# Performance work log

Hardware: AMD Instinct MI355X
Metric: run time of the kernel (lower is better)

The kernel has to match this reference:

```python
import jax, jax.numpy as jnp
import numpy as np

N = 10000        # nodes
F_IN = 128       # node features (data.num_node_features)
OUT = 16         # out_channels
H = 32           # attention heads
C1 = 4 * OUT     # hidden per-head dim (4*out_channels)
E = 80000        # directed edges
EPS = 1e-5       # BatchNorm eps
NEG = 0.2        # GATConv LeakyReLU negative_slope


def _gat(x, src, dst, W, a_s, a_d, b, n, C):
    # PyG GATConv, shared lin, concat=False (mean over heads)
    h = (x @ W).reshape(n, H, C)                    # [n,H,C]
    e_src = jnp.sum(h * a_s, -1)                    # [n,H] (alpha from x_j)
    e_dst = jnp.sum(h * a_d, -1)                    # [n,H] (alpha from x_i)
    e = jax.nn.leaky_relu(e_src[src] + e_dst[dst], NEG)     # [E',H]
    m = jax.ops.segment_max(e, dst, num_segments=n)         # segment softmax
    p = jnp.exp(e - m[dst])
    z = jax.ops.segment_sum(p, dst, num_segments=n)
    alpha = p / z[dst]
    out = jax.ops.segment_sum(alpha[:, :, None] * h[src], dst, num_segments=n)
    return out.mean(1) + b                          # mean over heads + bias


def _bn(x, g, b, m, v):  # eval-mode BatchNorm1d (running stats)
    return (x - m) * g / jnp.sqrt(v + EPS) + b


def setup_inputs():
    k = jax.random.split(jax.random.key(0), 40)
    rn = lambda i, s, sc=0.1: jax.random.normal(k[i], s, jnp.float32) * sc
    d = {"x": jax.random.normal(k[0], (N, F_IN), jnp.float32),
         "edge_index": jax.random.randint(k[1], (2, E), 0, N, jnp.int32)}
    # 4 GATConv layers
    d.update(W1=rn(2, (F_IN, H * C1)), as1=rn(3, (H, C1)), ad1=rn(4, (H, C1)), b1=rn(5, (C1,)))
    d.update(W2=rn(6, (C1, H * OUT)), as2=rn(7, (H, OUT)), ad2=rn(8, (H, OUT)), b2=rn(9, (OUT,)))
    d.update(W3=rn(10, (F_IN, H * C1)), as3=rn(11, (H, C1)), ad3=rn(12, (H, C1)), b3=rn(13, (C1,)))
    d.update(W4=rn(14, (C1, H * OUT)), as4=rn(15, (H, OUT)), ad4=rn(16, (H, OUT)), b4=rn(17, (OUT,)))
    # ResidualNetwork(1 block): 1x1 Conv1d over L=1 == matmul
    d.update(rwa=rn(18, (F_IN, OUT)), rba=rn(19, (OUT,)),
             bn1g=jnp.ones(OUT), bn1b=jnp.zeros(OUT), bn1m=rn(20, (OUT,)), bn1v=jnp.abs(rn(21, (OUT,))) + 1.0,
             rwb=rn(22, (OUT, OUT)), rbb=rn(23, (OUT,)),
             bn2g=jnp.ones(OUT), bn2b=jnp.zeros(OUT), bn2m=rn(24, (OUT,)), bn2v=jnp.abs(rn(25, (OUT,))) + 1.0,
             wsc=rn(26, (F_IN, OUT)), bsc=rn(27, (OUT,)),
             bnsg=jnp.ones(OUT), bnsb=jnp.zeros(OUT), bnsm=rn(28, (OUT,)), bnsv=jnp.abs(rn(29, (OUT,))) + 1.0,
             wfc=rn(30, (OUT, OUT)), bfc=rn(31, (OUT,)))
    return d


def reference(x, edge_index, W1, as1, ad1, b1, W2, as2, ad2, b2,
              W3, as3, ad3, b3, W4, as4, ad4, b4,
              rwa, rba, bn1g, bn1b, bn1m, bn1v, rwb, rbb, bn2g, bn2b, bn2m, bn2v,
              wsc, bsc, bnsg, bnsb, bnsm, bnsv, wfc, bfc):
    n = x.shape[0]
    loops = jnp.arange(n, dtype=edge_index.dtype)  # add_self_loops=True
    s2t_src = jnp.concatenate([edge_index[0], loops])  # flow source_to_target
    s2t_dst = jnp.concatenate([edge_index[1], loops])
    t2s_src = jnp.concatenate([edge_index[1], loops])  # flow target_to_source
    t2s_dst = jnp.concatenate([edge_index[0], loops])
    # dropout in original is unassigned (no-op); eval mode assumed
    x_s = jax.nn.elu(_gat(x, s2t_src, s2t_dst, W1, as1, ad1, b1, n, C1))
    x_in = jax.nn.elu(_gat(x_s, s2t_src, s2t_dst, W2, as2, ad2, b2, n, OUT))
    x_t = jax.nn.elu(_gat(x, t2s_src, t2s_dst, W3, as3, ad3, b3, n, C1))
    x_out = jax.nn.elu(_gat(x_t, t2s_src, t2s_dst, W4, as4, ad4, b4, n, OUT))
    # ResidualNetwork: block + identity avg-pool (L=1) + fc
    h = jax.nn.relu(_bn(x @ rwa + rba, bn1g, bn1b, bn1m, bn1v))
    h = _bn(h @ rwb + rbb, bn2g, bn2b, bn2m, bn2v)
    sc = _bn(x @ wsc + bsc, bnsg, bnsb, bnsm, bnsv)
    x_self = jax.nn.relu(h + sc) @ wfc + bfc
    return (x_in, x_out, x_self)
```

## Files before the change

### kernel.cpp

```cpp
#include <hip/hip_runtime.h>
#include <stdint.h>

__device__ __forceinline__ float bf2f(unsigned short u) {
  union { unsigned int i; float f; } v; v.i = ((unsigned int)u) << 16; return v.f;
}
__device__ __forceinline__ unsigned short f2bf(float f) {
  union { float f; unsigned int i; } v; v.f = f;
  unsigned int i = v.i;
  unsigned int r = (i + 0x7fffu + ((i >> 16) & 1u)) >> 16;
  return (unsigned short)r;
}

typedef __bf16 bf16x8 __attribute__((ext_vector_type(8)));
typedef float f32x4 __attribute__((ext_vector_type(4)));
typedef float f32x2 __attribute__((ext_vector_type(2)));
union ABfrag { int4 i4; bf16x8 v; };

#if __has_builtin(__builtin_amdgcn_cvt_pk_fp8_f32) && __has_builtin(__builtin_amdgcn_cvt_pk_f32_fp8)
#define HW_FP8 1
#else
#define HW_FP8 0
#endif

__device__ __forceinline__ unsigned char f2fp8_sw(float f) {
  union { float f; unsigned int u; } v; v.f = f;
  unsigned int s = (v.u >> 24) & 0x80;
  float a = fabsf(f);
  if (a >= 448.f) return (unsigned char)(s | 0x7E);
  v.f = a;
  int ex = (int)(v.u >> 23);
  unsigned int man = v.u & 0x7FFFFFu;
  if (ex >= 121) {
    unsigned int val = ((unsigned int)(ex - 120) << 3) | (man >> 20);
    unsigned int rem = man & 0xFFFFFu;
    if (rem > 0x80000u || (rem == 0x80000u && (val & 1))) val++;
    if (val > 0x7E) val = 0x7E;
    return (unsigned char)(s | val);
  }
  int q = (int)(a * 512.f + 0.5f);
  if (q > 8) q = 8;
  return (unsigned char)(s | (unsigned int)q);
}
__device__ __forceinline__ float fp8dec_sw(unsigned char c) {
  unsigned int e = (c >> 3) & 15u, m = c & 7u;
  float v;
  if (e) { union { unsigned int u; float f; } x; x.u = ((e + 120) << 23) | (m << 20); v = x.f; }
  else v = (float)m * 0.001953125f;
  return (c & 0x80) ? -v : v;
}
__device__ __forceinline__ unsigned int pack4_fp8(float a0, float a1, float a2, float a3) {
#if HW_FP8
  int dw = __builtin_amdgcn_cvt_pk_fp8_f32(a0, a1, 0, false);
  dw = __builtin_amdgcn_cvt_pk_fp8_f32(a2, a3, dw, true);
  return (unsigned int)dw;
#else
  return (unsigned)f2fp8_sw(a0) | ((unsigned)f2fp8_sw(a1) << 8) |
         ((unsigned)f2fp8_sw(a2) << 16) | ((unsigned)f2fp8_sw(a3) << 24);
#endif
}
__device__ __forceinline__ unsigned int bytesel4(uint4 v, int rr) {
#if __has_builtin(__builtin_amdgcn_perm)
  unsigned s = (unsigned)rr | ((unsigned)(rr + 4) << 8);
  unsigned p01 = __builtin_amdgcn_perm(v.y, v.x, s);
  unsigned p23 = __builtin_amdgcn_perm(v.w, v.z, s);
  return __builtin_amdgcn_perm(p23, p01, 0x05040100u);
#else
  int sh = rr * 8;
  return ((v.x >> sh) & 0xFFu) | (((v.y >> sh) & 0xFFu) << 8) |
         (((v.z >> sh) & 0xFFu) << 16) | (((v.w >> sh) & 0xFFu) << 24);
#endif
}
__device__ __forceinline__ void dec16p(int4 g, f32x2 o[8]) {
#if HW_FP8
  o[0] = __builtin_amdgcn_cvt_pk_f32_fp8(g.x, false);
  o[1] = __builtin_amdgcn_cvt_pk_f32_fp8(g.x, true);
  o[2] = __builtin_amdgcn_cvt_pk_f32_fp8(g.y, false);
  o[3] = __builtin_amdgcn_cvt_pk_f32_fp8(g.y, true);
  o[4] = __builtin_amdgcn_cvt_pk_f32_fp8(g.z, false);
  o[5] = __builtin_amdgcn_cvt_pk_f32_fp8(g.z, true);
  o[6] = __builtin_amdgcn_cvt_pk_f32_fp8(g.w, false);
  o[7] = __builtin_amdgcn_cvt_pk_f32_fp8(g.w, true);
#else
  unsigned int w[4] = {(unsigned)g.x, (unsigned)g.y, (unsigned)g.z, (unsigned)g.w};
#pragma unroll
  for (int d = 0; d < 4; ++d) {
    unsigned int x = w[d];
    o[d * 2 + 0] = (f32x2){fp8dec_sw((unsigned char)(x & 0xFF)),
                           fp8dec_sw((unsigned char)((x >> 8) & 0xFF))};
    o[d * 2 + 1] = (f32x2){fp8dec_sw((unsigned char)((x >> 16) & 0xFF)),
                           fp8dec_sw((unsigned char)((x >> 24) & 0xFF))};
  }
#endif
}

__device__ __forceinline__ float lrelu_clamp(float e) {
  e = (e > 0.f) ? e : 0.2f * e;
  return fminf(e, 80.f);
}

__global__ __launch_bounds__(256) void k_detect(const unsigned int* __restrict__ x, int* flag,
                                                int* __restrict__ degAB, int ndeg2) {
  if (blockIdx.x == 0) {
    __shared__ int cnt;
    if (threadIdx.x == 0) cnt = 0;
    __syncthreads();
    int c = 0;
    for (int i = threadIdx.x; i < 1024; i += 256) {
      unsigned int lo = x[i] & 0xFFFFu;
      int ex = (int)((lo >> 7) & 0xFF);
      if (ex >= 100 && ex <= 140) c++;
    }
    atomicAdd(&cnt, c);
    __syncthreads();
    if (threadIdx.x == 0) flag[0] = (cnt > 600) ? 1 : 0;
    return;
  }
  for (int idx = (blockIdx.x - 1) * 256 + threadIdx.x; idx < ndeg2; idx += 8 * 256) degAB[idx] = 0;
}

struct PrepDesc {
  const void* csrc[32]; float* cdst[32]; int cn[32];
  const void* x; float* xc; unsigned short* xp;
  const void* W1; const void* W2; const void* W3; const void* W4;
  unsigned short* P1; unsigned short* P2; unsigned short* P3; unsigned short* P4;
  int* degAB;
  const int* ei;
  const void* av[4];
  float* wa[4];
  int nxb, xtotal, ctotal, E, nn;
};
__global__ __launch_bounds__(256) void k_prep(PrepDesc d, const int* __restrict__ flag) {
  int isbf = *flag;
  int b = blockIdx.x;
  if (b < d.nxb) {
    int t8 = b * 256 + threadIdx.x;
    int i8 = t8 * 8;
    if (i8 < d.xtotal) {
      float v[8];
      if (isbf) {
        int4 raw = *(const int4*)((const unsigned short*)d.x + i8);
        const unsigned short* u = (const unsigned short*)&raw;
#pragma unroll
        for (int j = 0; j < 8; ++j) v[j] = bf2f(u[j]);
      } else {
        float4 f0 = *(const float4*)((const float*)d.x + i8);
        float4 f1 = *(const float4*)((const float*)d.x + i8 + 4);
        v[0] = f0.x; v[1] = f0.y; v[2] = f0.z; v[3] = f0.w;
        v[4] = f1.x; v[5] = f1.y; v[6] = f1.z; v[7] = f1.w;
      }
      *(float4*)(d.xc + i8)     = (float4){v[0], v[1], v[2], v[3]};
      *(float4*)(d.xc + i8 + 4) = (float4){v[4], v[5], v[6], v[7]};
      int row = i8 >> 7, c0 = i8 & 127;
      int tm = row >> 4, mr = row & 15;
      int s = c0 >> 5, quad = (c0 >> 3) & 3;
      unsigned short o[8];
#pragma unroll
      for (int j = 0; j < 8; ++j) o[j] = f2bf(v[j]);
      size_t idx = (((size_t)tm * 4 + s) * 64 + quad * 16 + mr) * 8;
      *(int4*)(d.xp + idx) = *(const int4*)o;
    }
    return;
  }
  b -= d.nxb;
  if (b < 288) {
    int u = b * 256 + threadIdx.x;
    const void* W; unsigned short* P; int K, N, lu;
    if (u < 32768)      { W = d.W1; P = d.P1; K = 128; N = 2048; lu = u; }
    else if (u < 36864) { W = d.W2; P = d.P2; K = 64;  N = 512;  lu = u - 32768; }
    else if (u < 69632) { W = d.W3; P = d.P3; K = 128; N = 2048; lu = u - 36864; }
    else                { W = d.W4; P = d.P4; K = 64;  N = 512;  lu = u - 69632; }
    int ksteps = K >> 5;
    int g = lu / (ksteps * 64);
    int rem = lu - g * (ksteps * 64);
    int s = rem >> 6, lane = rem & 63;
    int mr = lane & 15, quad = lane >> 4;
    int col = g * 16 + mr;
    int kbase = s * 32 + quad * 8;
#pragma unroll
    for (int j = 0; j < 8; ++j) {
      size_t src = (size_t)(kbase + j) * N + col;
      float v = isbf ? bf2f(((const unsigned short*)W)[src]) : ((const float*)W)[src];
      P[(size_t)lu * 8 + j] = f2bf(v);
    }
    return;
  }
  b -= 288;
  if (b < 4) {
    for (int idx = b * 256 + threadIdx.x; idx < d.ctotal; idx += 4 * 256) {
      int t = 0, off = idx;
      while (off >= d.cn[t]) { off -= d.cn[t]; ++t; }
      float v = isbf ? bf2f(((const unsigned short*)d.csrc[t])[off])
                     : ((const float*)d.csrc[t])[off];
      d.cdst[t][off] = v;
    }
    return;
  }
  b -= 4;
  {
    int degblks = (d.E + 255) >> 8;
    if (b < degblks) {
      int e = b * 256 + threadIdx.x;
      if (e < d.E) {
        atomicAdd(&d.degAB[d.ei[d.E + e]], 1);
        atomicAdd(&d.degAB[d.nn + d.ei[e]], 1);
      }
      return;
    }
    b -= degblks;
  }
  {
    int m = b >> 4, kb = b & 15;
    const void* W = (m < 2) ? d.W1 : d.W3;
    const void* A = d.av[m];
    float* out = d.wa[m];
    int k = kb * 8 + (threadIdx.x >> 5);
    int h = threadIdx.x & 31;
    size_t wbase = (size_t)k * 2048 + h * 64;
    size_t abase = (size_t)h * 64;
    float acc = 0.f;
    if (isbf) {
      const unsigned short* Wb = (const unsigned short*)W;
      const unsigned short* Ab = (const unsigned short*)A;
#pragma unroll
      for (int v8 = 0; v8 < 8; ++v8) {
        int4 wv = *(const int4*)(Wb + wbase + v8 * 8);
        int4 av = *(const int4*)(Ab + abase + v8 * 8);
        const unsigned short* wu = (const unsigned short*)&wv;
        const unsigned short* au = (const unsigned short*)&av;
#pragma unroll
        for (int j = 0; j < 8; ++j) acc += bf2f(wu[j]) * bf2f(au[j]);
      }
    } else {
      const float* Wf = (const float*)W;
      const float* Af = (const float*)A;
#pragma unroll
      for (int v4 = 0; v4 < 16; ++v4) {
        float4 wv = *(const float4*)(Wf + wbase + v4 * 4);
        float4 av = *(const float4*)(Af + abase + v4 * 4);
        acc += wv.x * av.x + wv.y * av.y + wv.z * av.z + wv.w * av.w;
      }
    }
    out[k * 32 + h] = acc;
  }
}

__global__ __launch_bounds__(1024) void k_exscan2(const int* __restrict__ degA, const int* __restrict__ degB,
                                                  int* __restrict__ rowA, int* __restrict__ rowB,
                                                  int* __restrict__ colA, int* __restrict__ colB,
                                                  int* __restrict__ curA, int* __restrict__ curB, int n) {
  const int* deg = (blockIdx.x == 0) ? degA : degB;
  int* row = (blockIdx.x == 0) ? rowA : rowB;
  int* colx = (blockIdx.x == 0) ? colA : colB;
  int* curx = (blockIdx.x == 0) ? curA : curB;
  __shared__ int wsum[16], wbase[16];
  __shared__ int carry;
  if (threadIdx.x == 0) carry = 0;
  __syncthreads();
  int lane = threadIdx.x & 63, w = threadIdx.x >> 6;
  int chunks = (n + 1023) >> 10;
  for (int ch = 0; ch < chunks; ++ch) {
    int i = (ch << 10) + threadIdx.x;
    int v = (i < n) ? deg[i] : 0;
    int sc = v;
#pragma unroll
    for (int o = 1; o < 64; o <<= 1) { int t = __shfl_up(sc, o); if (lane >= o) sc += t; }
    if (lane == 63) wsum[w] = sc;
    __syncthreads();
    if (threadIdx.x < 16) {
      int v2 = wsum[threadIdx.x], s2 = v2;
#pragma unroll
      for (int o = 1; o < 16; o <<= 1) { int t = __shfl_up(s2, o); if (lane >= o) s2 += t; }
      wbase[threadIdx.x] = s2 - v2;
      if (threadIdx.x == 15) wsum[15] = s2;
    }
    __syncthreads();
    if (i < n) {
      int rv = carry + wbase[w] + (sc - v) + i;
      row[i] = rv;
      colx[rv] = i;
      curx[i] = rv + 1;
    }
    __syncthreads();
    if (threadIdx.x == 0) carry += wsum[15];
    __syncthreads();
  }
  if (threadIdx.x == 0) row[n] = carry + n;
}

struct AuxDesc {
  int resblks, E;
  const int* ei; int* colA; int* colB; int* curA; int* curB;
  const float* xc;
  const float* rp[20];
  const float* wa[4];
  float* es1; float* ed1; float* es3; float* ed3;
  void* outbase; size_t eoff; int n;
  const int* flag;
};
__global__ __launch_bounds__(256) void k_aux(AuxDesc d) {
  __shared__ struct { float xs[16][128]; float ha[16][16]; float tt[16][16]; } sm;
  int b = blockIdx.x;
  if (b < d.resblks) {
    int nodebase = b * 16;
    for (int t = threadIdx.x; t < 16 * 128; t += 256)
      sm.xs[t >> 7][t & 127] = d.xc[(size_t)(nodebase + (t >> 7)) * 128 + (t & 127)];
    __syncthreads();
    int ni = threadIdx.x >> 4, c = threadIdx.x & 15;
    {
      const float* w0 = d.wa[0]; const float* w1 = d.wa[1];
      const float* w2 = d.wa[2]; const float* w3 = d.wa[3];
      float a0 = 0.f, a1 = 0.f, a2 = 0.f, a3 = 0.f, a4 = 0.f, a5 = 0.f, a6 = 0.f, a7 = 0.f;
#pragma unroll 4
      for (int k = 0; k < 128; ++k) {
        float xv = sm.xs[ni][k];
        int o = k * 32 + c;
        a0 += xv * w0[o]; a1 += xv * w0[o + 16];
        a2 += xv * w1[o]; a3 += xv * w1[o + 16];
        a4 += xv * w2[o]; a5 += xv * w2[o + 16];
        a6 += xv * w3[o]; a7 += xv * w3[o + 16];
      }
      int row = nodebase + ni;
      d.es1[row * 32 + c] = a0; d.es1[row * 32 + c + 16] = a1;
      d.ed1[row * 32 + c] = a2; d.ed1[row * 32 + c + 16] = a3;
      d.es3[row * 32 + c] = a4; d.es3[row * 32 + c + 16] = a5;
      d.ed3[row * 32 + c] = a6; d.ed3[row * 32 + c + 16] = a7;
    }
    const float* rwa = d.rp[0]; const float* rba = d.rp[1];
    const float* bn1g = d.rp[2]; const float* bn1b = d.rp[3];
    const float* bn1m = d.rp[4]; const float* bn1v = d.rp[5];
    const float* rwb = d.rp[6]; const float* rbb = d.rp[7];
    const float* bn2g = d.rp[8]; const float* bn2b = d.rp[9];
    const float* bn2m = d.rp[10]; const float* bn2v = d.rp[11];
    const float* wsc = d.rp[12]; const float* bsc = d.rp[13];
    const float* bnsg = d.rp[14]; const float* bnsb = d.rp[15];
    const float* bnsm = d.rp[16]; const float* bnsv = d.rp[17];
    const float* wfc = d.rp[18]; const float* bfc = d.rp[19];
    float ya = 0.f, ysc = 0.f;
#pragma unroll 8
    for (int k = 0; k < 128; ++k) {
      float xv = sm.xs[ni][k];
      ya  += xv * rwa[k * 16 + c];
      ysc += xv * wsc[k * 16 + c];
    }
    ya += rba[c]; ysc += bsc[c];
    float s1 = bn1g[c] * rsqrtf(bn1v[c] + 1e-5f);
    ya = (ya - bn1m[c]) * s1 + bn1b[c];
    ya = fmaxf(ya, 0.f);
    float ss = bnsg[c] * rsqrtf(bnsv[c] + 1e-5f);
    ysc = (ysc - bnsm[c]) * ss + bnsb[c];
    sm.ha[ni][c] = ya;
    __syncthreads();
    float h2 = rbb[c];
#pragma unroll
    for (int k = 0; k < 16; ++k) h2 += sm.ha[ni][k] * rwb[k * 16 + c];
    float s2 = bn2g[c] * rsqrtf(bn2v[c] + 1e-5f);
    h2 = (h2 - bn2m[c]) * s2 + bn2b[c];
    sm.tt[ni][c] = fmaxf(h2 + ysc, 0.f);
    __syncthreads();
    float o = bfc[c];
#pragma unroll
    for (int k = 0; k < 16; ++k) o += sm.tt[ni][k] * wfc[k * 16 + c];
    size_t oo = d.eoff + (size_t)(nodebase + ni) * 16 + c;
    if (*d.flag) ((unsigned short*)d.outbase)[oo] = f2bf(o);
    else         ((float*)d.outbase)[oo] = o;
    return;
  }
  b -= d.resblks;
  {
    int e = b * 256 + threadIdx.x;
    if (e < d.E) {
      int s = d.ei[e], dd = d.ei[d.E + e];
      d.colA[atomicAdd(&d.curA[dd], 1)] = s;
      d.colB[atomicAdd(&d.curB[s], 1)] = dd;
    }
  }
}

#define TILE_DW 288
template<int CH, int KSTEPS>
__device__ __forceinline__ void mm_es64_body(int rg, int cg, int MT,
    const unsigned short* __restrict__ Ap, const unsigned short* __restrict__ Bp,
    unsigned char* __restrict__ C, const float* __restrict__ a_s, const float* __restrict__ a_d,
    float* __restrict__ es, float* __restrict__ ed, int N, unsigned int* tile) {
  const int TI = KSTEPS * 64;
  int vt = MT - rg * 4; if (vt > 4) vt = 4;
  int wid = threadIdx.x >> 6;
  int tn = cg * 4 + wid;
  int lane = threadIdx.x & 63;
  int mr = lane & 15, quad = lane >> 4;
  const int4* ap = (const int4*)(Ap + (size_t)rg * 4 * TI * 8) + lane;
  const unsigned short* bp = Bp + ((size_t)tn * 4 * KSTEPS) * 512 + lane * 8;
  unsigned int* twave = tile + wid * TILE_DW;
  f32x4 acc[4][4];
#pragma unroll
  for (int rt = 0; rt < 4; ++rt)
#pragma unroll
    for (int nt = 0; nt < 4; ++nt) acc[rt][nt] = (f32x4){0.f, 0.f, 0.f, 0.f};
#pragma unroll
  for (int s = 0; s < KSTEPS; ++s) {
    ABfrag bfr[4];
#pragma unroll
    for (int nt = 0; nt < 4; ++nt) bfr[nt].i4 = *(const int4*)(bp + (size_t)(nt * KSTEPS + s) * 512);
    ABfrag afr[4];
#pragma unroll
    for (int rt = 0; rt < 4; ++rt) {
      int rti = (rt < vt) ? rt : 0;
      afr[rt].i4 = ap[rti * TI + s * 64];
    }
#pragma unroll
    for (int nt = 0; nt < 4; ++nt)
#pragma unroll
      for (int rt = 0; rt < 4; ++rt)
        acc[rt][nt] = __builtin_amdgcn_mfma_f32_16x16x32_bf16(afr[rt].v, bfr[nt].v, acc[rt][nt], 0, 0, 0);
  }
  int r16 = lane >> 2, seg = lane & 3;
  int qr = r16 >> 2, rr = r16 & 3;
#pragma unroll
  for (int rt = 0; rt < 4; ++rt) {
    if (rt < vt) {
      int tm = rg * 4 + rt;
#pragma unroll
      for (int nt = 0; nt < 4; ++nt) {
        unsigned int dwv = pack4_fp8(acc[rt][nt][0], acc[rt][nt][1], acc[rt][nt][2], acc[rt][nt][3]);
        twave[quad * 72 + nt * 16 + mr] = dwv;
      }
      unsigned int out[4];
#pragma unroll
      for (int w = 0; w < 4; ++w) {
        uint4 v = *(const uint4*)&twave[qr * 72 + seg * 16 + 4 * w];
        out[w] = bytesel4(v, rr);
      }
      *(int4*)(C + (size_t)(tm * 16 + r16) * N + tn * 64 + seg * 16) = *(const int4*)out;
    }
  }
  if (CH == 16) {
    float ws[4], wd[4];
#pragma unroll
    for (int nt = 0; nt < 4; ++nt) {
      ws[nt] = a_s[(tn * 4 + nt) * 16 + mr];
      wd[nt] = a_d[(tn * 4 + nt) * 16 + mr];
    }
#pragma unroll
    for (int rt = 0; rt < 4; ++rt) {
      if (rt < vt) {
        int tm = rg * 4 + rt;
        float pes[4][4], ped[4][4];
#pragma unroll
        for (int nt = 0; nt < 4; ++nt)
#pragma unroll
          for (int r = 0; r < 4; ++r) { pes[nt][r] = acc[rt][nt][r] * ws[nt]; ped[nt][r] = acc[rt][nt][r] * wd[nt]; }
#pragma unroll
        for (int m = 1; m < 16; m <<= 1)
#pragma unroll
          for (int nt = 0; nt < 4; ++nt)
#pragma unroll
            for (int r = 0; r < 4; ++r) {
              pes[nt][r] += __shfl_xor(pes[nt][r], m);
              ped[nt][r] += __shfl_xor(ped[nt][r], m);
            }
        if (mr == 0) {
#pragma unroll
          for (int nt = 0; nt < 4; ++nt)
#pragma unroll
            for (int r = 0; r < 4; ++r) {
              int row = tm * 16 + quad * 4 + r;
              es[row * 32 + tn * 4 + nt] = pes[nt][r];
              ed[row * 32 + tn * 4 + nt] = ped[nt][r];
            }
        }
      }
    }
  }
}

struct MMDesc {
  const unsigned short* Ap;
  const unsigned short* B1; const unsigned short* B3;
  unsigned char* C1; unsigned char* C3;
  int mmblks, mt;
};
__global__ __launch_bounds__(256) void k_mm13(MMDesc d) {
  __shared__ unsigned int tile[4 * TILE_DW];
  int b = blockIdx.x;
  if (b < d.mmblks) {
    mm_es64_body<64,4>(b >> 3, b & 7, d.mt, d.Ap, d.B1, d.C1, nullptr, nullptr, nullptr, nullptr, 2048, tile);
    return;
  }
  b -= d.mmblks;
  mm_es64_body<64,4>(b >> 3, b & 7, d.mt, d.Ap, d.B3, d.C3, nullptr, nullptr, nullptr, nullptr, 2048, tile);
}

__global__ __launch_bounds__(256) void k_g64(const unsigned char* __restrict__ h1,
                                             const unsigned char* __restrict__ h3,
                                             const float* __restrict__ es1, const float* __restrict__ ed1,
                                             const float* __restrict__ es3, const float* __restrict__ ed3,
                                             const int* __restrict__ rowA, const int* __restrict__ colA,
                                             const int* __restrict__ rowB, const int* __restrict__ colB,
                                             const float* __restrict__ b1, const float* __restrict__ b3,
                                             unsigned short* __restrict__ xsp, unsigned short* __restrict__ xtp,
                                             int n, int gb) {
  int b = blockIdx.x;
  const unsigned char* h; const float *es, *ed, *bias; const int *rowp, *col; unsigned short* outp;
  if (b < gb) { h = h1; es = es1; ed = ed1; rowp = rowA; col = colA; bias = b1; outp = xsp; }
  else { b -= gb; h = h3; es = es3; ed = ed3; rowp = rowB; col = colB; bias = b3; outp = xtp; }
  int wid = threadIdx.x >> 6, lane = threadIdx.x & 63;
  int i = b * 4 + wid;
  if (i >= n) return;
  int hd0 = lane >> 2, hd1 = 16 + hd0;
  float e0 = ed[i * 32 + hd0];
  float e1 = ed[i * 32 + hd1];
  int beg = rowp[i], end = rowp[i + 1];
  int deg = end - beg;
  int colv = (lane < deg) ? col[beg + lane] : 0;
  f32x2 acc0[8], acc1[8];
#pragma unroll
  for (int k = 0; k < 8; ++k) { acc0[k] = (f32x2){0.f, 0.f}; acc1[k] = (f32x2){0.f, 0.f}; }
  float Z0 = 0.f, Z1 = 0.f;
  int s0 = __shfl(colv, 0);
  const int4* hp0 = (const int4*)(h + (size_t)s0 * 2048);
  int4 ng0 = hp0[lane];
  int4 ng1 = hp0[64 + lane];
  float na = es[s0 * 32 + hd0];
  float nb = es[s0 * 32 + hd1];
  for (int j = 0; j < deg; ++j) {
    int4 g0 = ng0, g1 = ng1;
    float ea = na, eb = nb;
    int jn = j + 1;
    if (jn < deg) {
      int sn = (jn < 64) ? __shfl(colv, jn) : col[beg + jn];
      const int4* hq = (const int4*)(h + (size_t)sn * 2048);
      ng0 = hq[lane];
      ng1 = hq[64 + lane];
      na = es[sn * 32 + hd0];
      nb = es[sn * 32 + hd1];
    }
    float q0 = __expf(lrelu_clamp(ea + e0));
    float q1 = __expf(lrelu_clamp(eb + e1));
    Z0 += q0; Z1 += q1;
    f32x2 d0[8], d1[8];
    dec16p(g0, d0); dec16p(g1, d1);
    f32x2 q0v = (f32x2){q0, q0}, q1v = (f32x2){q1, q1};
#pragma unroll
    for (int k = 0; k < 8; ++k) {
      acc0[k] = __builtin_elementwise_fma(q0v, d0[k], acc0[k]);
      acc1[k] = __builtin_elementwise_fma(q1v, d1[k], acc1[k]);
    }
  }
  float zi0 = 1.0f / Z0, zi1 = 1.0f / Z1;
  f32x2 zi0v = (f32x2){zi0, zi0}, zi1v = (f32x2){zi1, zi1};
  f32x2 v2[8];
#pragma unroll
  for (int k = 0; k < 8; ++k)
    v2[k] = __builtin_elementwise_fma(acc1[k], zi1v, acc0[k] * zi0v);
#pragma unroll
  for (int m = 4; m < 64; m <<= 1)
#pragma unroll
    for (int k = 0; k < 8; ++k) {
      v2[k].x += __shfl_xor(v2[k].x, m);
      v2[k].y += __shfl_xor(v2[k].y, m);
    }
  if (lane < 4) {
    float v[16];
#pragma unroll
    for (int k = 0; k < 8; ++k) { v[2 * k] = v2[k].x; v[2 * k + 1] = v2[k].y; }
    int tm = i >> 4, mr = i & 15;
    unsigned short ob[16];
#pragma unroll
    for (int k = 0; k < 16; ++k) {
      float t = v[k] * (1.f / 32.f) + bias[lane * 16 + k];
      t = (t > 0.f) ? t : (__expf(t) - 1.f);
      ob[k] = f2bf(t);
    }
    int s0w = lane >> 1;
#pragma unroll
    for (int g2 = 0; g2 < 2; ++g2) {
      size_t idx = (((size_t)tm * 2 + s0w) * 64 + ((lane & 1) * 2 + g2) * 16 + mr) * 8;
      *(int4*)(outp + idx) = *(const int4*)(ob + g2 * 8);
    }
  }
}

__global__ __launch_bounds__(256) void k_mm24(const unsigned short* __restrict__ xsp,
                                              const unsigned short* __restrict__ xtp,
                                              const unsigned short* __restrict__ W2p,
                                              const unsigned short* __restrict__ W4p,
                                              unsigned char* __restrict__ h2, unsigned char* __restrict__ h4,
                                              const float* __restrict__ as2, const float* __restrict__ ad2,
                                              const float* __restrict__ as4, const float* __restrict__ ad4,
                                              float* __restrict__ es2, float* __restrict__ ed2,
                                              float* __restrict__ es4, float* __restrict__ ed4,
                                              int mmblks, int mt) {
  __shared__ unsigned int tile[4 * TILE_DW];
  int b = blockIdx.x;
  if (b < mmblks)
    mm_es64_body<16,2>(b >> 1, b & 1, mt, xsp, W2p, h2, as2, ad2, es2, ed2, 512, tile);
  else {
    b -= mmblks;
    mm_es64_body<16,2>(b >> 1, b & 1, mt, xtp, W4p, h4, as4, ad4, es4, ed4, 512, tile);
  }
}

__global__ __launch_bounds__(256) void k_g16(const unsigned char* __restrict__ h2,
                                             const unsigned char* __restrict__ h4,
                                             const float* __restrict__ es2, const float* __restrict__ ed2,
                                             const float* __restrict__ es4, const float* __restrict__ ed4,
                                             const int* __restrict__ rowA, const int* __restrict__ colA,
                                             const int* __restrict__ rowB, const int* __restrict__ colB,
                                             const float* __restrict__ b2, const float* __restrict__ b4,
                                             void* __restrict__ outbase, int n, int gb,
                                             const int* __restrict__ flag) {
  int b = blockIdx.x;
  const unsigned char* h; const float *es, *ed, *bias; const int *rowp, *col; size_t eoff;
  if (b < gb) { h = h2; es = es2; ed = ed2; rowp = rowA; col = colA; bias = b2; eoff = 0; }
  else { b -= gb; h = h4; es = es4; ed = ed4; rowp = rowB; col = colB; bias = b4; eoff = (size_t)n * 16; }
  int wid = threadIdx.x >> 6, lane = threadIdx.x & 63;
  int i = b * 4 + wid;
  if (i >= n) return;
  int hh = lane & 31, j2 = lane >> 5;
  float ev = ed[i * 32 + hh];
  int beg = rowp[i], end = rowp[i + 1];
  int deg = end - beg;
  int colv = (lane < deg) ? col[beg + lane] : 0;
  f32x2 acc[8];
#pragma unroll
  for (int k = 0; k < 8; ++k) acc[k] = (f32x2){0.f, 0.f};
  float Z = 0.f;
  int j = j2;
  int4 ng = (int4){0, 0, 0, 0};
  float ne = 0.f;
  if (j < deg) {
    int s = __shfl(colv, j);
    ng = ((const int4*)(h + (size_t)s * 512))[hh];
    ne = es[s * 32 + hh];
  }
  for (; j < deg; j += 2) {
    int4 g = ng; float ee = ne;
    int jn = j + 2;
    if (jn < deg) {
      int sn = (jn < 64) ? __shfl(colv, jn) : col[beg + jn];
      ng = ((const int4*)(h + (size_t)sn * 512))[hh];
      ne = es[sn * 32 + hh];
    }
    float q = __expf(lrelu_clamp(ee + ev));
    Z += q;
    f32x2 d[8];
    dec16p(g, d);
    f32x2 qv = (f32x2){q, q};
#pragma unroll
    for (int k = 0; k < 8; ++k) acc[k] = __builtin_elementwise_fma(qv, d[k], acc[k]);
  }
  Z += __shfl_xor(Z, 32);
  float zi = 1.0f / Z;
  f32x2 ziv = (f32x2){zi, zi};
  f32x2 v2[8];
#pragma unroll
  for (int k = 0; k < 8; ++k) v2[k] = acc[k] * ziv;
#pragma unroll
  for (int m = 1; m < 64; m <<= 1)
#pragma unroll
    for (int k = 0; k < 8; ++k) {
      v2[k].x += __shfl_xor(v2[k].x, m);
      v2[k].y += __shfl_xor(v2[k].y, m);
    }
  if (lane == 0) {
    float v[16];
#pragma unroll
    for (int k = 0; k < 8; ++k) { v[2 * k] = v2[k].x; v[2 * k + 1] = v2[k].y; }
    int isbf = *flag;
    if (isbf) {
      unsigned short ob[16];
#pragma unroll
      for (int k = 0; k < 16; ++k) {
        float t = v[k] * (1.f / 32.f) + bias[k];
        t = (t > 0.f) ? t : (__expf(t) - 1.f);
        ob[k] = f2bf(t);
      }
      unsigned short* o = (unsigned short*)outbase + eoff + (size_t)i * 16;
      *(int4*)o = *(const int4*)ob;
      *(int4*)(o + 8) = *(const int4*)(ob + 8);
    } else {
      float* o = (float*)outbase + eoff + (size_t)i * 16;
#pragma unroll
      for (int k = 0; k < 16; ++k) {
        float t = v[k] * (1.f / 32.f) + bias[k];
        t = (t > 0.f) ? t : (__expf(t) - 1.f);
        o[k] = t;
      }
    }
  }
}

extern "C" void kernel_launch(void* const* d_in, const int* in_sizes, int n_in,
                              void* d_out, int out_size, void* d_ws, size_t ws_size,
                              hipStream_t stream) {
  const int n = in_sizes[0] / 128;
  const int E = in_sizes[1] / 2;
  const int* ei = (const int*)d_in[1];

  char* wsp = (char*)d_ws; size_t off = 0;
  auto alloc = [&](size_t bytes) -> void* {
    void* p = wsp + off; off = (off + bytes + 255) & ~(size_t)255; return p;
  };
  int* flag = (int*)alloc(4);
  float* xc = (float*)alloc((size_t)n * 128 * 4);
  unsigned short* xp = (unsigned short*)alloc((size_t)n * 128 * 2);
  unsigned short* W1p = (unsigned short*)alloc((size_t)2048 * 128 * 2);
  unsigned short* W2p = (unsigned short*)alloc((size_t)512 * 64 * 2);
  unsigned short* W3p = (unsigned short*)alloc((size_t)2048 * 128 * 2);
  unsigned short* W4p = (unsigned short*)alloc((size_t)512 * 64 * 2);
  unsigned char* h1 = (unsigned char*)alloc((size_t)n * 2048);
  unsigned char* h3 = (unsigned char*)alloc((size_t)n * 2048);
  unsigned char* h2 = (unsigned char*)alloc((size_t)n * 512);
  unsigned char* h4 = (unsigned char*)alloc((size_t)n * 512);
  float* es1 = (float*)alloc((size_t)n * 32 * 4);
  float* ed1 = (float*)alloc((size_t)n * 32 * 4);
  float* es3 = (float*)alloc((size_t)n * 32 * 4);
  float* ed3 = (float*)alloc((size_t)n * 32 * 4);
  float* es2 = (float*)alloc((size_t)n * 32 * 4);
  float* ed2 = (float*)alloc((size_t)n * 32 * 4);
  float* es4 = (float*)alloc((size_t)n * 32 * 4);
  float* ed4 = (float*)alloc((size_t)n * 32 * 4);
  unsigned short* xsp = (unsigned short*)alloc((size_t)n * 64 * 2);
  unsigned short* xtp = (unsigned short*)alloc((size_t)n * 64 * 2);
  int* rowA = (int*)alloc((size_t)(n + 1) * 4);
  int* rowB = (int*)alloc((size_t)(n + 1) * 4);
  int* colA = (int*)alloc((size_t)(E + n) * 4);
  int* colB = (int*)alloc((size_t)(E + n) * 4);
  int* degAB = (int*)alloc((size_t)2 * n * 4);
  int* degA = degAB, * degB = degAB + n;
  int* curA = (int*)alloc((size_t)n * 4);
  int* curB = (int*)alloc((size_t)n * 4);
  float* was1 = (float*)alloc((size_t)128 * 32 * 4);
  float* wad1 = (float*)alloc((size_t)128 * 32 * 4);
  float* was3 = (float*)alloc((size_t)128 * 32 * 4);
  float* wad3 = (float*)alloc((size_t)128 * 32 * 4);

  static const int cidx[32] = {3,4,5, 7,8,9, 11,12,13, 15,16,17,
                               18,19,20,21,22,23,24,25,26,27,28,29,
                               30,31,32,33,34,35,36,37};
  PrepDesc pd;
  float* canon[38] = {nullptr};
  pd.ctotal = 0;
  for (int t = 0; t < 32; ++t) {
    int ii = cidx[t];
    canon[ii] = (float*)alloc((size_t)in_sizes[ii] * 4);
    pd.csrc[t] = d_in[ii];
    pd.cdst[t] = canon[ii];
    pd.cn[t] = in_sizes[ii];
    pd.ctotal += in_sizes[ii];
  }
  pd.x = d_in[0]; pd.xc = xc; pd.xp = xp;
  pd.W1 = d_in[2]; pd.W2 = d_in[6]; pd.W3 = d_in[10]; pd.W4 = d_in[14];
  pd.P1 = W1p; pd.P2 = W2p; pd.P3 = W3p; pd.P4 = W4p;
  pd.degAB = degAB;
  pd.ei = ei;
  pd.av[0] = d_in[3]; pd.av[1] = d_in[4]; pd.av[2] = d_in[11]; pd.av[3] = d_in[12];
  pd.wa[0] = was1; pd.wa[1] = wad1; pd.wa[2] = was3; pd.wa[3] = wad3;
  pd.nxb = (n * 128 / 8 + 255) / 256;
  pd.xtotal = n * 128;
  pd.E = E;
  pd.nn = n;
  (void)ws_size; (void)n_in; (void)out_size;

  const int degblks = (E + 255) / 256;

  k_detect<<<9, 256, 0, stream>>>((const unsigned int*)d_in[0], flag, degAB, 2 * n);
  k_prep<<<pd.nxb + 288 + 4 + degblks + 64, 256, 0, stream>>>(pd, flag);
  k_exscan2<<<2, 1024, 0, stream>>>(degA, degB, rowA, rowB, colA, colB, curA, curB, n);

  const int mt = n / 16;
  const int nrg = (mt + 3) / 4;
  const int mmblks64 = nrg * 8;
  const int mmblks16 = nrg * 2;
  const int gb = (n + 3) / 4;

  AuxDesc ad;
  ad.resblks = mt; ad.E = E;
  ad.ei = ei; ad.colA = colA; ad.colB = colB; ad.curA = curA; ad.curB = curB;
  ad.xc = xc;
  for (int t = 0; t < 20; ++t) ad.rp[t] = canon[18 + t];
  ad.wa[0] = was1; ad.wa[1] = wad1; ad.wa[2] = was3; ad.wa[3] = wad3;
  ad.es1 = es1; ad.ed1 = ed1; ad.es3 = es3; ad.ed3 = ed3;
  ad.outbase = d_out; ad.eoff = (size_t)2 * n * 16; ad.n = n; ad.flag = flag;
  k_aux<<<mt + degblks, 256, 0, stream>>>(ad);

  MMDesc md;
  md.Ap = xp; md.B1 = W1p; md.B3 = W3p; md.C1 = h1; md.C3 = h3;
  md.mmblks = mmblks64; md.mt = mt;
  k_mm13<<<2 * mmblks64, 256, 0, stream>>>(md);

  k_g64<<<2 * gb, 256, 0, stream>>>(h1, h3, es1, ed1, es3, ed3,
                                    rowA, colA, rowB, colB,
                                    canon[5], canon[13], xsp, xtp, n, gb);
  k_mm24<<<2 * mmblks16, 256, 0, stream>>>(xsp, xtp, W2p, W4p, h2, h4,
                                           canon[7], canon[8], canon[15], canon[16],
                                           es2, ed2, es4, ed4, mmblks16, mt);
  k_g16<<<2 * gb, 256, 0, stream>>>(h2, h4, es2, ed2, es4, ed4,
                                    rowA, colA, rowB, colB,
                                    canon[9], canon[17], d_out, n, gb, flag);
}
```

Baseline: 324.8 us.

## Merge aux and projection kernels; double-buffer neighbor gathers in attention kernels

Folds the residual-network/edge-scatter kernel and the layer-1/3 matmul kernel into one launch, with the two sharing shared memory through a union. This removes a launch and lets the independent blocks run concurrently. The attention logits for heads c and c+16 are stored interleaved so each gather needs one float2 load instead of two scalar loads. Both aggregation kernels now keep two neighbors in flight (A/B ping-pong buffers) to hide gather latency, at the cost of more registers.

```diff
diff --git a/kernel.cpp b/kernel.cpp
--- a/kernel.cpp
+++ b/kernel.cpp
@@ -287,95 +287,6 @@
   if (threadIdx.x == 0) row[n] = carry + n;
 }
 
-struct AuxDesc {
-  int resblks, E;
-  const int* ei; int* colA; int* colB; int* curA; int* curB;
-  const float* xc;
-  const float* rp[20];
-  const float* wa[4];
-  float* es1; float* ed1; float* es3; float* ed3;
-  void* outbase; size_t eoff; int n;
-  const int* flag;
-};
-__global__ __launch_bounds__(256) void k_aux(AuxDesc d) {
-  __shared__ struct { float xs[16][128]; float ha[16][16]; float tt[16][16]; } sm;
-  int b = blockIdx.x;
-  if (b < d.resblks) {
-    int nodebase = b * 16;
-    for (int t = threadIdx.x; t < 16 * 128; t += 256)
-      sm.xs[t >> 7][t & 127] = d.xc[(size_t)(nodebase + (t >> 7)) * 128 + (t & 127)];
-    __syncthreads();
-    int ni = threadIdx.x >> 4, c = threadIdx.x & 15;
-    {
-      const float* w0 = d.wa[0]; const float* w1 = d.wa[1];
-      const float* w2 = d.wa[2]; const float* w3 = d.wa[3];
-      float a0 = 0.f, a1 = 0.f, a2 = 0.f, a3 = 0.f, a4 = 0.f, a5 = 0.f, a6 = 0.f, a7 = 0.f;
-#pragma unroll 4
-      for (int k = 0; k < 128; ++k) {
-        float xv = sm.xs[ni][k];
-        int o = k * 32 + c;
-        a0 += xv * w0[o]; a1 += xv * w0[o + 16];
-        a2 += xv * w1[o]; a3 += xv * w1[o + 16];
-        a4 += xv * w2[o]; a5 += xv * w2[o + 16];
-        a6 += xv * w3[o]; a7 += xv * w3[o + 16];
-      }
-      int row = nodebase + ni;
-      d.es1[row * 32 + c] = a0; d.es1[row * 32 + c + 16] = a1;
-      d.ed1[row * 32 + c] = a2; d.ed1[row * 32 + c + 16] = a3;
-      d.es3[row * 32 + c] = a4; d.es3[row * 32 + c + 16] = a5;
-      d.ed3[row * 32 + c] = a6; d.ed3[row * 32 + c + 16] = a7;
-    }
-    const float* rwa = d.rp[0]; const float* rba = d.rp[1];
-    const float* bn1g = d.rp[2]; const float* bn1b = d.rp[3];
-    const float* bn1m = d.rp[4]; const float* bn1v = d.rp[5];
-    const float* rwb = d.rp[6]; const float* rbb = d.rp[7];
-    const float* bn2g = d.rp[8]; const float* bn2b = d.rp[9];
-    const float* bn2m = d.rp[10]; const float* bn2v = d.rp[11];
-    const float* wsc = d.rp[12]; const float* bsc = d.rp[13];
-    const float* bnsg = d.rp[14]; const float* bnsb = d.rp[15];
-    const float* bnsm = d.rp[16]; const float* bnsv = d.rp[17];
-    const float* wfc = d.rp[18]; const float* bfc = d.rp[19];
-    float ya = 0.f, ysc = 0.f;
-#pragma unroll 8
-    for (int k = 0; k < 128; ++k) {
-      float xv = sm.xs[ni][k];
-      ya  += xv * rwa[k * 16 + c];
-      ysc += xv * wsc[k * 16 + c];
-    }
-    ya += rba[c]; ysc += bsc[c];
-    float s1 = bn1g[c] * rsqrtf(bn1v[c] + 1e-5f);
-    ya = (ya - bn1m[c]) * s1 + bn1b[c];
-    ya = fmaxf(ya, 0.f);
-    float ss = bnsg[c] * rsqrtf(bnsv[c] + 1e-5f);
-    ysc = (ysc - bnsm[c]) * ss + bnsb[c];
-    sm.ha[ni][c] = ya;
-    __syncthreads();
-    float h2 = rbb[c];
-#pragma unroll
-    for (int k = 0; k < 16; ++k) h2 += sm.ha[ni][k] * rwb[k * 16 + c];
-    float s2 = bn2g[c] * rsqrtf(bn2v[c] + 1e-5f);
-    h2 = (h2 - bn2m[c]) * s2 + bn2b[c];
-    sm.tt[ni][c] = fmaxf(h2 + ysc, 0.f);
-    __syncthreads();
-    float o = bfc[c];
-#pragma unroll
-    for (int k = 0; k < 16; ++k) o += sm.tt[ni][k] * wfc[k * 16 + c];
-    size_t oo = d.eoff + (size_t)(nodebase + ni) * 16 + c;
-    if (*d.flag) ((unsigned short*)d.outbase)[oo] = f2bf(o);
-    else         ((float*)d.outbase)[oo] = o;
-    return;
-  }
-  b -= d.resblks;
-  {
-    int e = b * 256 + threadIdx.x;
-    if (e < d.E) {
-      int s = d.ei[e], dd = d.ei[d.E + e];
-      d.colA[atomicAdd(&d.curA[dd], 1)] = s;
-      d.colB[atomicAdd(&d.curB[s], 1)] = dd;
-    }
-  }
-}
-
 #define TILE_DW 288
 template<int CH, int KSTEPS>
 __device__ __forceinline__ void mm_es64_body(int rg, int cg, int MT,
@@ -473,21 +384,108 @@
   }
 }
 
-struct MMDesc {
+union SM13 {
+  struct { float xs[16][128]; float ha[16][16]; float tt[16][16]; } res;
+  unsigned int tile[4 * TILE_DW];
+};
+struct MM13XDesc {
+  int resblks, sblks, mmblks, mt, E;
+  const int* ei; int* colA; int* colB; int* curA; int* curB;
+  const float* xc;
+  const float* rp[20];
+  const float* wa[4];
+  float* es1; float* ed1; float* es3; float* ed3;
+  void* outbase; size_t eoff; int n;
+  const int* flag;
   const unsigned short* Ap;
   const unsigned short* B1; const unsigned short* B3;
   unsigned char* C1; unsigned char* C3;
-  int mmblks, mt;
 };
-__global__ __launch_bounds__(256) void k_mm13(MMDesc d) {
-  __shared__ unsigned int tile[4 * TILE_DW];
+__global__ __launch_bounds__(256) void k_mm13x(MM13XDesc d) {
+  __shared__ SM13 sm;
   int b = blockIdx.x;
+  if (b < d.resblks) {
+    int nodebase = b * 16;
+    for (int t = threadIdx.x; t < 16 * 128; t += 256)
+      sm.res.xs[t >> 7][t & 127] = d.xc[(size_t)(nodebase + (t >> 7)) * 128 + (t & 127)];
+    __syncthreads();
+    int ni = threadIdx.x >> 4, c = threadIdx.x & 15;
+    {
+      const float* w0 = d.wa[0]; const float* w1 = d.wa[1];
+      const float* w2 = d.wa[2]; const float* w3 = d.wa[3];
+      float a0 = 0.f, a1 = 0.f, a2 = 0.f, a3 = 0.f, a4 = 0.f, a5 = 0.f, a6 = 0.f, a7 = 0.f;
+#pragma unroll 4
+      for (int k = 0; k < 128; ++k) {
+        float xv = sm.res.xs[ni][k];
+        int o = k * 32 + c;
+        a0 += xv * w0[o]; a1 += xv * w0[o + 16];
+        a2 += xv * w1[o]; a3 += xv * w1[o + 16];
+        a4 += xv * w2[o]; a5 += xv * w2[o + 16];
+        a6 += xv * w3[o]; a7 += xv * w3[o + 16];
+      }
+      int row = nodebase + ni;
+      *(float2*)&d.es1[row * 32 + 2 * c] = (float2){a0, a1};
+      *(float2*)&d.ed1[row * 32 + 2 * c] = (float2){a2, a3};
+      *(float2*)&d.es3[row * 32 + 2 * c] = (float2){a4, a5};
+      *(float2*)&d.ed3[row * 32 + 2 * c] = (float2){a6, a7};
+    }
+    const float* rwa = d.rp[0]; const float* rba = d.rp[1];
+    const float* bn1g = d.rp[2]; const float* bn1b = d.rp[3];
+    const float* bn1m = d.rp[4]; const float* bn1v = d.rp[5];
+    const float* rwb = d.rp[6]; const float* rbb = d.rp[7];
+    const float* bn2g = d.rp[8]; const float* bn2b = d.rp[9];
+    const float* bn2m = d.rp[10]; const float* bn2v = d.rp[11];
+    const float* wsc = d.rp[12]; const float* bsc = d.rp[13];
+    const float* bnsg = d.rp[14]; const float* bnsb = d.rp[15];
+    const float* bnsm = d.rp[16]; const float* bnsv = d.rp[17];
+    const float* wfc = d.rp[18]; const float* bfc = d.rp[19];
+    float ya = 0.f, ysc = 0.f;
+#pragma unroll 8
+    for (int k = 0; k < 128; ++k) {
+      float xv = sm.res.xs[ni][k];
+      ya  += xv * rwa[k * 16 + c];
+      ysc += xv * wsc[k * 16 + c];
+    }
+    ya += rba[c]; ysc += bsc[c];
+    float s1 = bn1g[c] * rsqrtf(bn1v[c] + 1e-5f);
+    ya = (ya - bn1m[c]) * s1 + bn1b[c];
+    ya = fmaxf(ya, 0.f);
+    float ss = bnsg[c] * rsqrtf(bnsv[c] + 1e-5f);
+    ysc = (ysc - bnsm[c]) * ss + bnsb[c];
+    sm.res.ha[ni][c] = ya;
+    __syncthreads();
+    float h2 = rbb[c];
+#pragma unroll
+    for (int k = 0; k < 16; ++k) h2 += sm.res.ha[ni][k] * rwb[k * 16 + c];
+    float s2 = bn2g[c] * rsqrtf(bn2v[c] + 1e-5f);
+    h2 = (h2 - bn2m[c]) * s2 + bn2b[c];
+    sm.res.tt[ni][c] = fmaxf(h2 + ysc, 0.f);
+    __syncthreads();
+    float o = bfc[c];
+#pragma unroll
+    for (int k = 0; k < 16; ++k) o += sm.res.tt[ni][k] * wfc[k * 16 + c];
+    size_t oo = d.eoff + (size_t)(nodebase + ni) * 16 + c;
+    if (*d.flag) ((unsigned short*)d.outbase)[oo] = f2bf(o);
+    else         ((float*)d.outbase)[oo] = o;
+    return;
+  }
+  b -= d.resblks;
+  if (b < d.sblks) {
+    int e = b * 256 + threadIdx.x;
+    if (e < d.E) {
+      int s = d.ei[e], dd = d.ei[d.E + e];
+      d.colA[atomicAdd(&d.curA[dd], 1)] = s;
+      d.colB[atomicAdd(&d.curB[s], 1)] = dd;
+    }
+    return;
+  }
+  b -= d.sblks;
   if (b < d.mmblks) {
-    mm_es64_body<64,4>(b >> 3, b & 7, d.mt, d.Ap, d.B1, d.C1, nullptr, nullptr, nullptr, nullptr, 2048, tile);
+    mm_es64_body<64,4>(b >> 3, b & 7, d.mt, d.Ap, d.B1, d.C1, nullptr, nullptr, nullptr, nullptr, 2048, sm.tile);
     return;
   }
   b -= d.mmblks;
-  mm_es64_body<64,4>(b >> 3, b & 7, d.mt, d.Ap, d.B3, d.C3, nullptr, nullptr, nullptr, nullptr, 2048, tile);
+  mm_es64_body<64,4>(b >> 3, b & 7, d.mt, d.Ap, d.B3, d.C3, nullptr, nullptr, nullptr, nullptr, 2048, sm.tile);
 }
 
 __global__ __launch_bounds__(256) void k_g64(const unsigned char* __restrict__ h1,
@@ -506,9 +504,10 @@
   int wid = threadIdx.x >> 6, lane = threadIdx.x & 63;
   int i = b * 4 + wid;
   if (i >= n) return;
-  int hd0 = lane >> 2, hd1 = 16 + hd0;
-  float e0 = ed[i * 32 + hd0];
-  float e1 = ed[i * 32 + hd1];
+  int hd0 = lane >> 2;
+  const float2* esp = (const float2*)es;
+  const float2* edp = (const float2*)ed;
+  float2 e01 = edp[i * 16 + hd0];
   int beg = rowp[i], end = rowp[i + 1];
   int deg = end - beg;
   int colv = (lane < deg) ? col[beg + lane] : 0;
@@ -516,35 +515,61 @@
 #pragma unroll
   for (int k = 0; k < 8; ++k) { acc0[k] = (f32x2){0.f, 0.f}; acc1[k] = (f32x2){0.f, 0.f}; }
   float Z0 = 0.f, Z1 = 0.f;
-  int s0 = __shfl(colv, 0);
-  const int4* hp0 = (const int4*)(h + (size_t)s0 * 2048);
-  int4 ng0 = hp0[lane];
-  int4 ng1 = hp0[64 + lane];
-  float na = es[s0 * 32 + hd0];
-  float nb = es[s0 * 32 + hd1];
-  for (int j = 0; j < deg; ++j) {
-    int4 g0 = ng0, g1 = ng1;
-    float ea = na, eb = nb;
-    int jn = j + 1;
-    if (jn < deg) {
-      int sn = (jn < 64) ? __shfl(colv, jn) : col[beg + jn];
+  int sA = __shfl(colv, 0);
+  const int4* hp = (const int4*)(h + (size_t)sA * 2048);
+  int4 gA0 = hp[lane], gA1 = hp[64 + lane];
+  float2 eA = esp[sA * 16 + hd0];
+  int4 gB0 = gA0, gB1 = gA1; float2 eB = eA;
+  if (deg > 1) {
+    int sB = __shfl(colv, 1);
+    const int4* hq = (const int4*)(h + (size_t)sB * 2048);
+    gB0 = hq[lane]; gB1 = hq[64 + lane];
+    eB = esp[sB * 16 + hd0];
+  }
+  int j = 0;
+  while (true) {
+    {
+      float q0 = __expf(lrelu_clamp(eA.x + e01.x));
+      float q1 = __expf(lrelu_clamp(eA.y + e01.y));
+      Z0 += q0; Z1 += q1;
+      f32x2 d0[8], d1[8];
+      dec16p(gA0, d0); dec16p(gA1, d1);
+      f32x2 q0v = (f32x2){q0, q0}, q1v = (f32x2){q1, q1};
+#pragma unroll
+      for (int k = 0; k < 8; ++k) {
+        acc0[k] = __builtin_elementwise_fma(q0v, d0[k], acc0[k]);
+        acc1[k] = __builtin_elementwise_fma(q1v, d1[k], acc1[k]);
+      }
+    }
+    int jp = j + 2;
+    if (jp < deg) {
+      int sn = (jp < 64) ? __shfl(colv, jp) : col[beg + jp];
       const int4* hq = (const int4*)(h + (size_t)sn * 2048);
-      ng0 = hq[lane];
-      ng1 = hq[64 + lane];
-      na = es[sn * 32 + hd0];
-      nb = es[sn * 32 + hd1];
-    }
-    float q0 = __expf(lrelu_clamp(ea + e0));
-    float q1 = __expf(lrelu_clamp(eb + e1));
-    Z0 += q0; Z1 += q1;
-    f32x2 d0[8], d1[8];
-    dec16p(g0, d0); dec16p(g1, d1);
-    f32x2 q0v = (f32x2){q0, q0}, q1v = (f32x2){q1, q1};
-#pragma unroll
-    for (int k = 0; k < 8; ++k) {
-      acc0[k] = __builtin_elementwise_fma(q0v, d0[k], acc0[k]);
-      acc1[k] = __builtin_elementwise_fma(q1v, d1[k], acc1[k]);
-    }
+      gA0 = hq[lane]; gA1 = hq[64 + lane];
+      eA = esp[sn * 16 + hd0];
+    }
+    if (++j >= deg) break;
+    {
+      float q0 = __expf(lrelu_clamp(eB.x + e01.x));
+      float q1 = __expf(lrelu_clamp(eB.y + e01.y));
+      Z0 += q0; Z1 += q1;
+      f32x2 d0[8], d1[8];
+      dec16p(gB0, d0); dec16p(gB1, d1);
+      f32x2 q0v = (f32x2){q0, q0}, q1v = (f32x2){q1, q1};
+#pragma unroll
+      for (int k = 0; k < 8; ++k) {
+        acc0[k] = __builtin_elementwise_fma(q0v, d0[k], acc0[k]);
+        acc1[k] = __builtin_elementwise_fma(q1v, d1[k], acc1[k]);
+      }
+    }
+    jp = j + 2;
+    if (jp < deg) {
+      int sn = (jp < 64) ? __shfl(colv, jp) : col[beg + jp];
+      const int4* hq = (const int4*)(h + (size_t)sn * 2048);
+      gB0 = hq[lane]; gB1 = hq[64 + lane];
+      eB = esp[sn * 16 + hd0];
+    }
+    if (++j >= deg) break;
   }
   float zi0 = 1.0f / Z0, zi1 = 1.0f / Z1;
   f32x2 zi0v = (f32x2){zi0, zi0}, zi1v = (f32x2){zi1, zi1};
@@ -626,28 +651,52 @@
   for (int k = 0; k < 8; ++k) acc[k] = (f32x2){0.f, 0.f};
   float Z = 0.f;
   int j = j2;
-  int4 ng = (int4){0, 0, 0, 0};
-  float ne = 0.f;
+  int4 gA = (int4){0, 0, 0, 0}; float eA = 0.f;
   if (j < deg) {
     int s = __shfl(colv, j);
-    ng = ((const int4*)(h + (size_t)s * 512))[hh];
-    ne = es[s * 32 + hh];
-  }
-  for (; j < deg; j += 2) {
-    int4 g = ng; float ee = ne;
-    int jn = j + 2;
-    if (jn < deg) {
-      int sn = (jn < 64) ? __shfl(colv, jn) : col[beg + jn];
-      ng = ((const int4*)(h + (size_t)sn * 512))[hh];
-      ne = es[sn * 32 + hh];
-    }
-    float q = __expf(lrelu_clamp(ee + ev));
-    Z += q;
-    f32x2 d[8];
-    dec16p(g, d);
-    f32x2 qv = (f32x2){q, q};
-#pragma unroll
-    for (int k = 0; k < 8; ++k) acc[k] = __builtin_elementwise_fma(qv, d[k], acc[k]);
+    gA = ((const int4*)(h + (size_t)s * 512))[hh];
+    eA = es[s * 32 + hh];
+  }
+  int4 gB = (int4){0, 0, 0, 0}; float eB = 0.f;
+  if (j + 2 < deg) {
+    int s = __shfl(colv, j + 2);
+    gB = ((const int4*)(h + (size_t)s * 512))[hh];
+    eB = es[s * 32 + hh];
+  }
+  while (j < deg) {
+    {
+      float q = __expf(lrelu_clamp(eA + ev));
+      Z += q;
+      f32x2 d[8];
+      dec16p(gA, d);
+      f32x2 qv = (f32x2){q, q};
+#pragma unroll
+      for (int k = 0; k < 8; ++k) acc[k] = __builtin_elementwise_fma(qv, d[k], acc[k]);
+    }
+    int jp = j + 4;
+    if (jp < deg) {
+      int s = (jp < 64) ? __shfl(colv, jp) : col[beg + jp];
+      gA = ((const int4*)(h + (size_t)s * 512))[hh];
+      eA = es[s * 32 + hh];
+    }
+    j += 2;
+    if (j >= deg) break;
+    {
+      float q = __expf(lrelu_clamp(eB + ev));
+      Z += q;
+      f32x2 d[8];
+      dec16p(gB, d);
+      f32x2 qv = (f32x2){q, q};
+#pragma unroll
+      for (int k = 0; k < 8; ++k) acc[k] = __builtin_elementwise_fma(qv, d[k], acc[k]);
+    }
+    jp = j + 4;
+    if (jp < deg) {
+      int s = (jp < 64) ? __shfl(colv, jp) : col[beg + jp];
+      gB = ((const int4*)(h + (size_t)s * 512))[hh];
+      eB = es[s * 32 + hh];
+    }
+    j += 2;
   }
   Z += __shfl_xor(Z, 32);
   float zi = 1.0f / Z;
@@ -774,20 +823,16 @@
   const int mmblks16 = nrg * 2;
   const int gb = (n + 3) / 4;
 
-  AuxDesc ad;
-  ad.resblks = mt; ad.E = E;
-  ad.ei = ei; ad.colA = colA; ad.colB = colB; ad.curA = curA; ad.curB = curB;
-  ad.xc = xc;
-  for (int t = 0; t < 20; ++t) ad.rp[t] = canon[18 + t];
-  ad.wa[0] = was1; ad.wa[1] = wad1; ad.wa[2] = was3; ad.wa[3] = wad3;
-  ad.es1 = es1; ad.ed1 = ed1; ad.es3 = es3; ad.ed3 = ed3;
-  ad.outbase = d_out; ad.eoff = (size_t)2 * n * 16; ad.n = n; ad.flag = flag;
-  k_aux<<<mt + degblks, 256, 0, stream>>>(ad);
-
-  MMDesc md;
+  MM13XDesc md;
+  md.resblks = mt; md.sblks = degblks; md.mmblks = mmblks64; md.mt = mt; md.E = E;
+  md.ei = ei; md.colA = colA; md.colB = colB; md.curA = curA; md.curB = curB;
+  md.xc = xc;
+  for (int t = 0; t < 20; ++t) md.rp[t] = canon[18 + t];
+  md.wa[0] = was1; md.wa[1] = wad1; md.wa[2] = was3; md.wa[3] = wad3;
+  md.es1 = es1; md.ed1 = ed1; md.es3 = es3; md.ed3 = ed3;
+  md.outbase = d_out; md.eoff = (size_t)2 * n * 16; md.n = n; md.flag = flag;
   md.Ap = xp; md.B1 = W1p; md.B3 = W3p; md.C1 = h1; md.C3 = h3;
-  md.mmblks = mmblks64; md.mt = mt;
-  k_mm13<<<2 * mmblks64, 256, 0, stream>>>(md);
+  k_mm13x<<<mt + degblks + 2 * mmblks64, 256, 0, stream>>>(md);
 
   k_g64<<<2 * gb, 256, 0, stream>>>(h1, h3, es1, ed1, es3, ed3,
                                     rowA, colA, rowB, colB,
```

Result: no change. 320.9 us (-1.2%).
